# Kernel optimization log

Measured on AMD Instinct MI355X. Metric: run time of the kernel, lower is better.

Reference implementation:

```python
import jax, jax.numpy as jnp
import numpy as np

N, F, H, E, ES, G = 50000, 64, 4, 300000, 400000, 128
NS, EPS = 0.2, 1e-5  # LeakyReLU slope, BN eps


def setup_inputs() -> dict:
    k = jax.random.split(jax.random.key(0), 16)
    rn = lambda i, s, sc=1.0: jax.random.normal(k[i], s, jnp.float32) * sc
    return {
        "x": rn(0, (N, F)),
        "edge_index": jax.random.randint(k[1], (2, E), 0, N),
        "batch": jnp.sort(jax.random.randint(k[2], (N,), 0, G)),
        "scatter_edge_index": jax.random.randint(k[3], (4, 2, ES), 0, N),
        "scatter_edge_attr": rn(4, (4, ES), 0.1),
        "gat_W": rn(5, (4, F, H * F), 0.05),
        "gat_asrc": rn(6, (4, H, F), 0.05),
        "gat_adst": rn(7, (4, H, F), 0.05),
        "gat_bias": jnp.zeros((4, H * F)),
        "mlp_W": rn(8, (4, H * F, F), 0.05),
        "mlp_b": jnp.zeros((4, F)),
        "mlp_g": jnp.ones((4, F)), "mlp_beta": jnp.zeros((4, F)),
        "mlp_rm": jnp.zeros((4, F)), "mlp_rv": jax.random.uniform(k[9], (4, F)) + 0.5,
        "fc1_W": rn(10, (F, 256), 0.05), "fc1_b": jnp.zeros((256,)),
        "fc1_g": jnp.ones((256,)), "fc1_beta": jnp.zeros((256,)),
        "fc1_rm": jnp.zeros((256,)), "fc1_rv": jax.random.uniform(k[11], (256,)) + 0.5,
        "fc2_W": rn(12, (256, 64), 0.05), "fc2_b": jnp.zeros((64,)),
        "fc2_g": jnp.ones((64,)), "fc2_beta": jnp.zeros((64,)),
        "fc2_rm": jnp.zeros((64,)), "fc2_rv": jax.random.uniform(k[13], (64,)) + 0.5,
        "fc3_W": rn(14, (64, 10), 0.05), "fc3_b": jnp.zeros((10,)),
        "fc3_g": jnp.ones((10,)), "fc3_beta": jnp.zeros((10,)),
        "fc3_rm": jnp.zeros((10,)), "fc3_rv": jax.random.uniform(k[15], (10,)) + 0.5,
    }


def _bn(h, g, b, rm, rv):
    # BatchNorm1d in eval mode (running stats)
    return g * (h - rm) * jax.lax.rsqrt(rv + EPS) + b


def _forward(floats, ints):
    (x, sea, gW, gas, gad, gb, mW, mb, mg, mbe, mrm, mrv,
     f1W, f1b, f1g, f1be, f1rm, f1rv, f2W, f2b, f2g, f2be, f2rm, f2rv,
     f3W, f3b, f3g, f3be, f3rm, f3rv) = floats
    edge_index, batch, sei = ints
    n = x.shape[0]
    loop = jnp.arange(n)
    src = jnp.concatenate([edge_index[0], loop])  # GATConv adds self-loops
    dst = jnp.concatenate([edge_index[1], loop])

    def solo(i, h):
        # edge_attr-weighted scatter-add (solo_pass, aggr='add')
        s, t = sei[i, 0], sei[i, 1]
        return jax.ops.segment_sum(sea[i][:, None] * h[s], t, num_segments=n)

    def gat_mlp(i, h):
        hh = (h @ gW[i]).reshape(n, H, F)                       # [N,H,F]
        e = (hh * gas[i]).sum(-1)[src] + (hh * gad[i]).sum(-1)[dst]  # [E+N,H]
        e = jnp.where(e > 0, e, NS * e)                         # LeakyReLU(0.2)
        m = jax.ops.segment_max(e, dst, num_segments=n)         # segment softmax over dst
        ex = jnp.exp(e - m[dst])
        ssum = jax.ops.segment_sum(ex, dst, num_segments=n)
        alpha = ex / ssum[dst]
        out = jax.ops.segment_sum(hh[src] * alpha[:, :, None], dst, num_segments=n)
        out = out.reshape(n, H * F) + gb[i]                     # concat heads + bias
        h2 = jax.nn.elu(out) @ mW[i] + mb[i]                    # ELU -> Dropout(eval) -> Linear
        return _bn(h2, mg[i], mbe[i], mrm[i], mrv[i])

    x0 = solo(0, x)
    xh = [jnp.abs(solo(i, x)) for i in (1, 2, 3)]
    branches = [x0] + [solo(0, h) for h in xh]
    branches = [gat_mlp(i, branches[i]) for i in range(4)]
    x_stage2 = x + branches[0] + branches[1] + branches[2] + branches[3]
    pooled = jax.ops.segment_sum(x_stage2, batch, num_segments=G)   # global_add_pool
    h = jax.nn.relu(_bn(pooled @ f1W + f1b, f1g, f1be, f1rm, f1rv))
    h = jax.nn.relu(_bn(h @ f2W + f2b, f2g, f2be, f2rm, f2rv))
    return _bn(h @ f3W + f3b, f3g, f3be, f3rm, f3rv)  # [G, num_classes]


def reference(x, edge_index, batch, scatter_edge_index, scatter_edge_attr, gat_W, gat_asrc, gat_adst, gat_bias, mlp_W, mlp_b, mlp_g, mlp_beta, mlp_rm, mlp_rv, fc1_W, fc1_b, fc1_g, fc1_beta, fc1_rm, fc1_rv, fc2_W, fc2_b, fc2_g, fc2_beta, fc2_rm, fc2_rv, fc3_W, fc3_b, fc3_g, fc3_beta, fc3_rm, fc3_rv):
    floats = (x, scatter_edge_attr, gat_W, gat_asrc, gat_adst, gat_bias, mlp_W, mlp_b, mlp_g, mlp_beta, mlp_rm, mlp_rv, fc1_W, fc1_b, fc1_g, fc1_beta, fc1_rm, fc1_rv, fc2_W, fc2_b, fc2_g, fc2_beta, fc2_rm, fc2_rv, fc3_W, fc3_b, fc3_g, fc3_beta, fc3_rm, fc3_rv)
    return _forward(floats, (edge_index, batch, scatter_edge_index))
```

## Files before the change

### kernel.cpp

```cpp
#include <hip/hip_runtime.h>

typedef unsigned int uint;
typedef unsigned short u16;

#define NN 50000
#define FF 64
#define NHD 4
#define EE 300000
#define ESN 400000
#define NG 128
#define NSLOPE 0.2f
#define EPSBN 1e-5f

#define BINSZ 64
#define NBIN 782
#define NPOS (NBIN * BINSZ)
#define CHUNK 2048
#define NBLK 196
#define BST 40
#define BCAP 38

typedef float f32x4 __attribute__((ext_vector_type(4)));
typedef float f32x2 __attribute__((ext_vector_type(2)));
typedef short bf16x8 __attribute__((ext_vector_type(8)));
union U8 { uint4 u; bf16x8 s; };

static __device__ __forceinline__ float lrelu(float e) {
  return fmaxf(e, NSLOPE * e);
}
static __device__ __forceinline__ float bl(uint u) {
  return __uint_as_float(u << 16);
}
static __device__ __forceinline__ float bh(uint u) {
  return __uint_as_float(u & 0xFFFF0000u);
}
static __device__ __forceinline__ uint f2bf(float f) {
  uint u = __float_as_uint(f);
  return (u + 0x7FFFu + ((u >> 16) & 1u)) >> 16;
}
static __device__ __forceinline__ uint packbf(float a, float b) {
  return f2bf(a) | (f2bf(b) << 16);
}

__global__ __launch_bounds__(256) void k_setup(
    const float2* __restrict__ x, const float* __restrict__ gW,
    const float* __restrict__ gas, const float* __restrict__ gad,
    const float* __restrict__ mW, const float* __restrict__ mb,
    const float* __restrict__ mg, const float* __restrict__ mbe,
    const float* __restrict__ mrm, const float* __restrict__ mrv,
    uint* __restrict__ xbf, uint* __restrict__ WB2, float* __restrict__ wasd,
    uint* __restrict__ MB, float* __restrict__ cvec) {
  int i = blockIdx.x * 256 + threadIdx.x;
  if (i < NN * 32) {
    float2 v = x[i];
    xbf[i] = packbf(v.x, v.y);
  }
  int t = i;
  if (t < 8192) {
    int b = t >> 11, id = t & 2047;
    int h = id >> 9, r2 = id & 511;
    int q2 = r2 >> 8, r3 = r2 & 255;
    int ct = r3 >> 6, l = r3 & 63;
    int c = h * 64 + ct * 16 + (l & 15);
    int k0 = q2 * 32 + (l >> 4) * 8;
    const float* Wp = gW + b * 16384;
    uint4 o;
    o.x = packbf(Wp[(k0 + 0) * 256 + c], Wp[(k0 + 1) * 256 + c]);
    o.y = packbf(Wp[(k0 + 2) * 256 + c], Wp[(k0 + 3) * 256 + c]);
    o.z = packbf(Wp[(k0 + 4) * 256 + c], Wp[(k0 + 5) * 256 + c]);
    o.w = packbf(Wp[(k0 + 6) * 256 + c], Wp[(k0 + 7) * 256 + c]);
    ((uint4*)WB2)[t] = o;
  } else if (t < 8192 + 2048) {
    int id = t - 8192;
    int b = id >> 9, r = id & 511;
    int sd = r >> 8, r2 = r & 255;
    int h = r2 >> 6, k = r2 & 63;
    const float* Wp = gW + b * 16384;
    const float* ap = (sd ? gad : gas) + b * 256 + h * 64;
    float acc = 0.f;
    for (int f = 0; f < 64; ++f) acc += Wp[k * 256 + h * 64 + f] * ap[f];
    wasd[((b * 2 + sd) * 4 + h) * 64 + k] = acc;
  } else if (t < 8192 + 2048 + 8192) {
    int id = t - 10240;
    int b = id >> 11, rem = id & 2047;
    int tt = rem >> 6, l = rem & 63;
    int tile = tt >> 3, q2 = tt & 7;
    int c = tile * 16 + (l & 15);
    int k0 = q2 * 32 + (l >> 4) * 8;
    const float* Mp = mW + b * 16384;
    float sc = mg[b * 64 + c] * rsqrtf(mrv[b * 64 + c] + EPSBN);
    float v[8];
#pragma unroll
    for (int j = 0; j < 8; ++j) v[j] = Mp[(k0 + j) * 64 + c] * sc;
    uint4 o;
    o.x = packbf(v[0], v[1]); o.y = packbf(v[2], v[3]);
    o.z = packbf(v[4], v[5]); o.w = packbf(v[6], v[7]);
    ((uint4*)MB)[id] = o;
  } else if (t < 8192 + 2048 + 8192 + 64) {
    int c = t - 18432;
    float acc = 0.f;
#pragma unroll
    for (int b = 0; b < 4; ++b) {
      float sc = mg[b * 64 + c] * rsqrtf(mrv[b * 64 + c] + EPSBN);
      acc += sc * (mb[b * 64 + c] - mrm[b * 64 + c]) + mbe[b * 64 + c];
    }
    cvec[c] = acc;
  }
}

__global__ __launch_bounds__(256) void k_sort1(
    const int* __restrict__ sei, const float* __restrict__ sea,
    const int* __restrict__ ei, uint2* __restrict__ sorted,
    u16* __restrict__ offs) {
  __shared__ uint hist[NBIN];
  __shared__ uint wsum[4];
  __shared__ __align__(16) uint2 buf[CHUNK];
  int y = blockIdx.y, blk = blockIdx.x, tid = threadIdx.x;
  int E = (y < 4) ? ESN : EE;
  int e0 = blk * CHUNK;
  if (e0 >= E) return;
  int ec = E - e0; if (ec > CHUNK) ec = CHUNK;
  for (int i = tid; i < NBIN; i += 256) hist[i] = 0;
  __syncthreads();
  const int* sptr; const int* tptr; const float* wptr = 0;
  if (y < 4) {
    sptr = sei + (size_t)y * 2 * ESN; tptr = sptr + ESN;
    wptr = sea + (size_t)y * ESN;
  } else {
    sptr = ei; tptr = ei + EE;
  }
  uint2 rec[8]; uint rbin[8];
#pragma unroll
  for (int k = 0; k < 8; ++k) {
    int idx = tid + k * 256;
    rbin[k] = 0xFFFFFFFFu;
    if (idx < ec) {
      int e = e0 + idx;
      int s = sptr[e], t = tptr[e];
      uint w = (y < 4) ? (f2bf(wptr[e]) << 16) : 0u;
      rec[k].x = (uint)s | ((uint)(t & 63) << 16);
      rec[k].y = w;
      rbin[k] = (uint)(t >> 6);
      atomicAdd(&hist[rbin[k]], 1u);
    }
  }
  __syncthreads();
  int t4 = tid * 4;
  uint h0 = 0, h1 = 0, h2 = 0, h3 = 0;
  if (t4 + 0 < NBIN) h0 = hist[t4 + 0];
  if (t4 + 1 < NBIN) h1 = hist[t4 + 1];
  if (t4 + 2 < NBIN) h2 = hist[t4 + 2];
  if (t4 + 3 < NBIN) h3 = hist[t4 + 3];
  uint sl = h0 + h1 + h2 + h3;
  uint pre = sl;
#pragma unroll
  for (int off = 1; off < 64; off <<= 1) {
    uint nv = __shfl_up(pre, off);
    if ((tid & 63) >= off) pre += nv;
  }
  int wid = tid >> 6;
  if ((tid & 63) == 63) wsum[wid] = pre;
  __syncthreads();
  uint wbase = 0;
#pragma unroll
  for (int w = 0; w < 4; ++w) if (w < wid) wbase += wsum[w];
  uint base = wbase + pre - sl;
  if (t4 + 0 < NBIN) hist[t4 + 0] = base;
  if (t4 + 1 < NBIN) hist[t4 + 1] = base + h0;
  if (t4 + 2 < NBIN) hist[t4 + 2] = base + h0 + h1;
  if (t4 + 3 < NBIN) hist[t4 + 3] = base + h0 + h1 + h2;
  __syncthreads();
  u16* ob = offs + ((size_t)y * NBLK + blk) * 784;
  for (int i = tid; i < NBIN; i += 256) ob[i] = (u16)hist[i];
  if (tid == 0) { ob[NBIN] = (u16)ec; ob[NBIN + 1] = (u16)ec; }
  __syncthreads();
#pragma unroll
  for (int k = 0; k < 8; ++k) {
    if (rbin[k] != 0xFFFFFFFFu) {
      uint p = atomicAdd(&hist[rbin[k]], 1u);
      buf[p] = rec[k];
    }
  }
  __syncthreads();
  uint2* sb = sorted + ((size_t)y * NBLK + blk) * CHUNK;
  uint4* s4 = (uint4*)sb;
  const uint4* b4 = (const uint4*)buf;
  int n4 = (ec + 1) >> 1;
  for (int i = tid; i < n4; i += 256) s4[i] = b4[i];
}

__global__ __launch_bounds__(256) void k_sort2(
    const u16* __restrict__ offs, const uint2* __restrict__ sorted,
    uint* __restrict__ pbk, uint* __restrict__ gbk) {
  __shared__ __align__(16) uint Lb[BINSZ * BST];
  __shared__ uint Lc[BINSZ];
  __shared__ uint dh[64], dpos[64], sperm[64];
  int y = blockIdx.y, bin = blockIdx.x, tid = threadIdx.x;
  if (tid < BINSZ) Lc[tid] = 0u;
  if (tid < 64) dh[tid] = 0u;
  __syncthreads();
  int nblk = (y < 4) ? NBLK : 147;
  for (int sb = tid; sb < nblk; sb += 256) {
    const u16* ob = offs + ((size_t)y * NBLK + sb) * 784;
    uint st = ob[bin], en = ob[bin + 1];
    const uint2* src = sorted + ((size_t)y * NBLK + sb) * CHUNK;
    for (uint i = st; i < en; ++i) {
      uint2 r = src[i];
      uint tl = (r.x >> 16) & 63u;
      uint p = atomicAdd(&Lc[tl], 1u);
      if (p < BCAP) Lb[tl * BST + 2 + p] = (r.x & 0xFFFFu) | r.y;
    }
  }
  __syncthreads();
  uint myd = 0;
  if (tid < 64) {
    myd = Lc[tid]; if (myd > 63u) myd = 63u;
    atomicAdd(&dh[63u - myd], 1u);
  }
  __syncthreads();
  if (tid < 64) {
    uint v = dh[tid], p = v;
#pragma unroll
    for (int off = 1; off < 64; off <<= 1) {
      uint nv = __shfl_up(p, off);
      if (tid >= off) p += nv;
    }
    dpos[tid] = p - v;
  }
  __syncthreads();
  if (tid < 64) {
    uint slot = atomicAdd(&dpos[63u - myd], 1u);
    sperm[slot] = (uint)tid;
    Lb[tid * BST + 0] = Lc[tid];
    Lb[tid * BST + 1] = (uint)(bin * BINSZ + tid);
  }
  __syncthreads();
  uint* out = (y < 4) ? (pbk + ((size_t)y * NPOS + (size_t)bin * BINSZ) * BST)
                      : (gbk + (size_t)bin * BINSZ * BST);
  uint4* o4v = (uint4*)out;
  for (int i = tid; i < 64 * (BST / 4); i += 256) {
    int pos = i / (BST / 4), q = i % (BST / 4);
    uint sn = sperm[pos];
    uint4 v = *(const uint4*)&Lb[sn * BST + q * 4];
    o4v[(size_t)pos * (BST / 4) + q] = v;
  }
}

__global__ __launch_bounds__(256) void k_solo_gA(
    const uint* __restrict__ xbf, const uint* __restrict__ pbk,
    const float* __restrict__ wasd, uint* __restrict__ bbuf,
    uint* __restrict__ tmpb, float* __restrict__ es4,
    float* __restrict__ ed4) {
  int i = blockIdx.y;
  int tid = threadIdx.x;
  int pos = blockIdx.x * 32 + (tid >> 3);
  int sl = tid & 7;
  const uint* bk = pbk + ((size_t)i * NPOS + pos) * BST;
  int deg = (int)bk[0]; deg = deg > BCAP ? BCAP : deg;
  int id = (int)bk[1];
  if (id >= NN) return;
  const uint* pp = bk + 2;
  f32x2 A0 = {0.f, 0.f}, A1 = {0.f, 0.f}, A2 = {0.f, 0.f}, A3 = {0.f, 0.f};
  for (int j = 0; j < deg; j += 8) {
    uint2 pa = *(const uint2*)&pp[j];
    uint2 pb = *(const uint2*)&pp[j + 2];
    uint2 pc = *(const uint2*)&pp[j + 4];
    uint2 pd = *(const uint2*)&pp[j + 6];
    uint p0 = pa.x;
    uint p1 = (j + 1 < deg) ? pa.y : 0u;
    uint p2 = (j + 2 < deg) ? pb.x : 0u;
    uint p3 = (j + 3 < deg) ? pb.y : 0u;
    uint p4 = (j + 4 < deg) ? pc.x : 0u;
    uint p5 = (j + 5 < deg) ? pc.y : 0u;
    uint p6 = (j + 6 < deg) ? pd.x : 0u;
    uint p7 = (j + 7 < deg) ? pd.y : 0u;
    uint4 v0 = *(const uint4*)&xbf[(size_t)(p0 & 0xFFFFu) * 32 + sl * 4];
    uint4 v1 = *(const uint4*)&xbf[(size_t)(p1 & 0xFFFFu) * 32 + sl * 4];
    uint4 v2 = *(const uint4*)&xbf[(size_t)(p2 & 0xFFFFu) * 32 + sl * 4];
    uint4 v3 = *(const uint4*)&xbf[(size_t)(p3 & 0xFFFFu) * 32 + sl * 4];
    uint4 v4 = *(const uint4*)&xbf[(size_t)(p4 & 0xFFFFu) * 32 + sl * 4];
    uint4 v5 = *(const uint4*)&xbf[(size_t)(p5 & 0xFFFFu) * 32 + sl * 4];
    uint4 v6 = *(const uint4*)&xbf[(size_t)(p6 & 0xFFFFu) * 32 + sl * 4];
    uint4 v7 = *(const uint4*)&xbf[(size_t)(p7 & 0xFFFFu) * 32 + sl * 4];
#define SOLOA_EDGE(V, W)                              \
    {                                                 \
      float w_ = (W);                                 \
      f32x2 w2_ = {w_, w_};                           \
      A0 += (f32x2){bl(V.x), bh(V.x)} * w2_;          \
      A1 += (f32x2){bl(V.y), bh(V.y)} * w2_;          \
      A2 += (f32x2){bl(V.z), bh(V.z)} * w2_;          \
      A3 += (f32x2){bl(V.w), bh(V.w)} * w2_;          \
    }
    SOLOA_EDGE(v0, bh(p0));
    SOLOA_EDGE(v1, bh(p1));
    SOLOA_EDGE(v2, bh(p2));
    SOLOA_EDGE(v3, bh(p3));
    SOLOA_EDGE(v4, bh(p4));
    SOLOA_EDGE(v5, bh(p5));
    SOLOA_EDGE(v6, bh(p6));
    SOLOA_EDGE(v7, bh(p7));
#undef SOLOA_EDGE
  }
  uint4 o;
  o.x = packbf(A0[0], A0[1]); o.y = packbf(A1[0], A1[1]);
  o.z = packbf(A2[0], A2[1]); o.w = packbf(A3[0], A3[1]);
  if (i == 0) {
    *(uint4*)&bbuf[(size_t)id * 32 + sl * 4] = o;
  } else {
    *(uint4*)&tmpb[(size_t)id * 96 + (size_t)(i - 1) * 32 + sl * 4] = o;
  }
  if (i == 0) {
    float pv[8] = {A0[0], A0[1], A1[0], A1[1], A2[0], A2[1], A3[0], A3[1]};
    const float* wa = wasd;
    float r[8];
#pragma unroll
    for (int o8 = 0; o8 < 8; ++o8) {
      const float* w8 = wa + o8 * 64 + sl * 8;
      float a = 0.f;
#pragma unroll
      for (int j = 0; j < 8; ++j) a += pv[j] * w8[j];
      r[o8] = a;
    }
#pragma unroll
    for (int off = 1; off < 8; off <<= 1)
#pragma unroll
      for (int o8 = 0; o8 < 8; ++o8) r[o8] += __shfl_xor(r[o8], off);
    if (sl == 0) {
      *(float4*)&es4[(size_t)id * 4] = make_float4(r[0], r[1], r[2], r[3]);
      *(float4*)&ed4[(size_t)id * 4] = make_float4(r[4], r[5], r[6], r[7]);
    }
  }
}

__global__ __launch_bounds__(256) void k_solo_gB(
    const uint* __restrict__ tmpb, const uint* __restrict__ pbk,
    const float* __restrict__ wasd, uint* __restrict__ bbuf,
    float* __restrict__ es4, float* __restrict__ ed4) {
  int tid = threadIdx.x;
  int pos = blockIdx.x * 32 + (tid >> 3);
  int sl = tid & 7;
  const uint* bk = pbk + (size_t)pos * BST;
  int deg = (int)bk[0]; deg = deg > BCAP ? BCAP : deg;
  int id = (int)bk[1];
  if (id >= NN) return;
  const uint* pp = bk + 2;
  f32x2 A[3][4];
#pragma unroll
  for (int k = 0; k < 3; ++k)
#pragma unroll
    for (int c = 0; c < 4; ++c) A[k][c] = (f32x2){0.f, 0.f};
  for (int j = 0; j < deg; j += 4) {
    uint2 pa = *(const uint2*)&pp[j];
    uint2 pb = *(const uint2*)&pp[j + 2];
    uint p0 = pa.x;
    uint p1 = (j + 1 < deg) ? pa.y : 0u;
    uint p2 = (j + 2 < deg) ? pb.x : 0u;
    uint p3 = (j + 3 < deg) ? pb.y : 0u;
    const uint* b0 = &tmpb[(size_t)(p0 & 0xFFFFu) * 96 + sl * 4];
    const uint* b1 = &tmpb[(size_t)(p1 & 0xFFFFu) * 96 + sl * 4];
    const uint* b2 = &tmpb[(size_t)(p2 & 0xFFFFu) * 96 + sl * 4];
    const uint* b3 = &tmpb[(size_t)(p3 & 0xFFFFu) * 96 + sl * 4];
    uint4 v00 = *(const uint4*)&b0[0];
    uint4 v01 = *(const uint4*)&b0[32];
    uint4 v02 = *(const uint4*)&b0[64];
    uint4 v10 = *(const uint4*)&b1[0];
    uint4 v11 = *(const uint4*)&b1[32];
    uint4 v12 = *(const uint4*)&b1[64];
    uint4 v20 = *(const uint4*)&b2[0];
    uint4 v21 = *(const uint4*)&b2[32];
    uint4 v22 = *(const uint4*)&b2[64];
    uint4 v30 = *(const uint4*)&b3[0];
    uint4 v31 = *(const uint4*)&b3[32];
    uint4 v32 = *(const uint4*)&b3[64];
    float w0 = bh(p0), w1 = bh(p1), w2 = bh(p2), w3 = bh(p3);
    f32x2 w20 = {w0, w0}, w21 = {w1, w1}, w22 = {w2, w2}, w23 = {w3, w3};
#define SOLOB_EDGE(K, V, W)                                       \
    {                                                             \
      A[K][0] += (f32x2){fabsf(bl(V.x)), fabsf(bh(V.x))} * (W);   \
      A[K][1] += (f32x2){fabsf(bl(V.y)), fabsf(bh(V.y))} * (W);   \
      A[K][2] += (f32x2){fabsf(bl(V.z)), fabsf(bh(V.z))} * (W);   \
      A[K][3] += (f32x2){fabsf(bl(V.w)), fabsf(bh(V.w))} * (W);   \
    }
    SOLOB_EDGE(0, v00, w20); SOLOB_EDGE(1, v01, w20); SOLOB_EDGE(2, v02, w20);
    SOLOB_EDGE(0, v10, w21); SOLOB_EDGE(1, v11, w21); SOLOB_EDGE(2, v12, w21);
    SOLOB_EDGE(0, v20, w22); SOLOB_EDGE(1, v21, w22); SOLOB_EDGE(2, v22, w22);
    SOLOB_EDGE(0, v30, w23); SOLOB_EDGE(1, v31, w23); SOLOB_EDGE(2, v32, w23);
#undef SOLOB_EDGE
  }
#pragma unroll
  for (int k = 0; k < 3; ++k) {
    int b = k + 1;
    uint4 o;
    o.x = packbf(A[k][0][0], A[k][0][1]); o.y = packbf(A[k][1][0], A[k][1][1]);
    o.z = packbf(A[k][2][0], A[k][2][1]); o.w = packbf(A[k][3][0], A[k][3][1]);
    *(uint4*)&bbuf[(size_t)b * NN * 32 + (size_t)id * 32 + sl * 4] = o;
    float pv[8] = {A[k][0][0], A[k][0][1], A[k][1][0], A[k][1][1],
                   A[k][2][0], A[k][2][1], A[k][3][0], A[k][3][1]};
    const float* wa = wasd + b * 512;
    float r[8];
#pragma unroll
    for (int o8 = 0; o8 < 8; ++o8) {
      const float* w8 = wa + o8 * 64 + sl * 8;
      float a = 0.f;
#pragma unroll
      for (int j = 0; j < 8; ++j) a += pv[j] * w8[j];
      r[o8] = a;
    }
#pragma unroll
    for (int off = 1; off < 8; off <<= 1)
#pragma unroll
      for (int o8 = 0; o8 < 8; ++o8) r[o8] += __shfl_xor(r[o8], off);
    if (sl == 0) {
      *(float4*)&es4[(size_t)b * NN * 4 + (size_t)id * 4] =
          make_float4(r[0], r[1], r[2], r[3]);
      *(float4*)&ed4[(size_t)b * NN * 4 + (size_t)id * 4] =
          make_float4(r[4], r[5], r[6], r[7]);
    }
  }
}

__global__ __launch_bounds__(256) void k_agg(
    const uint* __restrict__ gbk, const float* __restrict__ es4,
    const float* __restrict__ ed4, const uint* __restrict__ bbuf,
    uint* __restrict__ agg4) {
  __shared__ uint gbr[32][40];
  __shared__ uint2 meta[32][32];
  int br = blockIdx.y;
  const float4* es44 = (const float4*)(es4 + (size_t)br * NN * 4);
  const float4* ed44 = (const float4*)(ed4 + (size_t)br * NN * 4);
  const uint* bbf = bbuf + (size_t)br * NN * 32;
  int tid = threadIdx.x;
  int p0 = blockIdx.x * 32;
  for (int idx = tid; idx < 320; idx += 256) {
    int i = idx / 10, q = idx % 10;
    *(uint4*)&gbr[i][q * 4] =
        *(const uint4*)&gbk[((size_t)p0 + i) * BST + q * 4];
  }
  __syncthreads();
  {
    int g = tid >> 5, hl = tid & 31;
#pragma unroll
    for (int rep = 0; rep < 4; ++rep) {
      int i = rep * 8 + g;
      int id = (int)gbr[i][1];
      bool vld = id < NN;
      int nds = vld ? id : 0;
      int deg = vld ? (int)gbr[i][0] : 0;
      deg = deg > 31 ? 31 : deg;
      int s0 = (hl < deg) ? (int)gbr[i][2 + hl] : nds;
      bool act = hl <= deg;
      float4 edd = ed44[nds];
      float4 e4 = es44[s0];
      float val[4];
      val[0] = act ? lrelu(e4.x + edd.x) : -3e38f;
      val[1] = act ? lrelu(e4.y + edd.y) : -3e38f;
      val[2] = act ? lrelu(e4.z + edd.z) : -3e38f;
      val[3] = act ? lrelu(e4.w + edd.w) : -3e38f;
      float m[4] = {val[0], val[1], val[2], val[3]};
#pragma unroll
      for (int off = 1; off < 32; off <<= 1)
#pragma unroll
        for (int h = 0; h < 4; ++h) m[h] = fmaxf(m[h], __shfl_xor(m[h], off));
      float e[4], sm[4];
#pragma unroll
      for (int h = 0; h < 4; ++h) {
        e[h] = act ? __expf(val[h] - m[h]) : 0.f;
        sm[h] = e[h];
      }
#pragma unroll
      for (int off = 1; off < 32; off <<= 1)
#pragma unroll
        for (int h = 0; h < 4; ++h) sm[h] += __shfl_xor(sm[h], off);
      float inv[4];
#pragma unroll
      for (int h = 0; h < 4; ++h) inv[h] = __builtin_amdgcn_rcpf(sm[h]);
      meta[i][hl] = make_uint2(packbf(e[0] * inv[0], e[1] * inv[1]),
                               packbf(e[2] * inv[2], e[3] * inv[3]));
    }
  }
  __syncthreads();
  {
    int wv = tid >> 6, l = tid & 63;
    int i = wv * 8 + (l >> 3), sl = l & 7;
    int id = (int)gbr[i][1];
    bool vld = id < NN;
    int self = vld ? id : 0;
    int deg = vld ? (int)gbr[i][0] : 0;
    deg = deg > 31 ? 31 : deg;
    int tot = deg + 1;
    f32x2 a00={0.f,0.f},a01={0.f,0.f},a02={0.f,0.f},a03={0.f,0.f};
    f32x2 a10={0.f,0.f},a11={0.f,0.f},a12={0.f,0.f},a13={0.f,0.f};
    f32x2 a20={0.f,0.f},a21={0.f,0.f},a22={0.f,0.f},a23={0.f,0.f};
    f32x2 a30={0.f,0.f},a31={0.f,0.f},a32={0.f,0.f},a33={0.f,0.f};
    for (int j = 0; j < tot; j += 4) {
      int s0 = (j     < deg) ? (int)gbr[i][2 + j]  : self;
      int s1 = (j + 1 < deg) ? (int)gbr[i][3 + j]  : self;
      int s2 = (j + 2 < deg) ? (int)gbr[i][4 + j]  : self;
      int s3 = (j + 3 < deg) ? (int)gbr[i][5 + j]  : self;
      uint2 al0 = meta[i][j];
      uint2 al1 = meta[i][j + 1];
      uint2 al2 = meta[i][j + 2];
      uint2 al3 = meta[i][j + 3];
      uint4 v0 = *(const uint4*)&bbf[(size_t)s0 * 32 + sl * 4];
      uint4 v1 = *(const uint4*)&bbf[(size_t)s1 * 32 + sl * 4];
      uint4 v2 = *(const uint4*)&bbf[(size_t)s2 * 32 + sl * 4];
      uint4 v3 = *(const uint4*)&bbf[(size_t)s3 * 32 + sl * 4];
#define AGG_EDGE(V, AL)                                              \
      {                                                              \
        f32x2 w0_={bl(AL.x),bl(AL.x)}, w1_={bh(AL.x),bh(AL.x)};      \
        f32x2 w2_={bl(AL.y),bl(AL.y)}, w3_={bh(AL.y),bh(AL.y)};      \
        f32x2 p0_={bl(V.x),bh(V.x)}, p1_={bl(V.y),bh(V.y)};          \
        f32x2 p2_={bl(V.z),bh(V.z)}, p3_={bl(V.w),bh(V.w)};          \
        a00+=p0_*w0_; a01+=p1_*w0_; a02+=p2_*w0_; a03+=p3_*w0_;      \
        a10+=p0_*w1_; a11+=p1_*w1_; a12+=p2_*w1_; a13+=p3_*w1_;      \
        a20+=p0_*w2_; a21+=p1_*w2_; a22+=p2_*w2_; a23+=p3_*w2_;      \
        a30+=p0_*w3_; a31+=p1_*w3_; a32+=p2_*w3_; a33+=p3_*w3_;      \
      }
      AGG_EDGE(v0, al0);
      AGG_EDGE(v1, al1);
      AGG_EDGE(v2, al2);
      AGG_EDGE(v3, al3);
#undef AGG_EDGE
    }
    if (vld) {
      uint* outp = agg4 + ((size_t)br * NN + id) * 128;
      uint4 o;
      o.x=packbf(a00[0],a00[1]); o.y=packbf(a01[0],a01[1]);
      o.z=packbf(a02[0],a02[1]); o.w=packbf(a03[0],a03[1]);
      *(uint4*)&outp[0 * 32 + sl * 4] = o;
      o.x=packbf(a10[0],a10[1]); o.y=packbf(a11[0],a11[1]);
      o.z=packbf(a12[0],a12[1]); o.w=packbf(a13[0],a13[1]);
      *(uint4*)&outp[1 * 32 + sl * 4] = o;
      o.x=packbf(a20[0],a20[1]); o.y=packbf(a21[0],a21[1]);
      o.z=packbf(a22[0],a22[1]); o.w=packbf(a23[0],a23[1]);
      *(uint4*)&outp[2 * 32 + sl * 4] = o;
      o.x=packbf(a30[0],a30[1]); o.y=packbf(a31[0],a31[1]);
      o.z=packbf(a32[0],a32[1]); o.w=packbf(a33[0],a33[1]);
      *(uint4*)&outp[3 * 32 + sl * 4] = o;
    }
  }
}

__global__ __launch_bounds__(256) void k_mlp2(
    const uint* __restrict__ agg4, const uint* __restrict__ WB2,
    const uint* __restrict__ MB4, const float* __restrict__ gb,
    const float* __restrict__ cvec, const float* __restrict__ xsrc,
    float* __restrict__ xs2) {
  __shared__ union UU2 {
    struct {
      uint astg[32][128];
      uint elu[4][32][32];
    } s;
    float red[4][32][64];
  } u;
  int tid = threadIdx.x, wv = tid >> 6, l = tid & 63;
  int quad = l >> 4, m16 = l & 15;
  int n0 = blockIdx.x * 32;
  int h = wv;
  f32x4 macc[2][4] = {{{0.f,0.f,0.f,0.f},{0.f,0.f,0.f,0.f},
                       {0.f,0.f,0.f,0.f},{0.f,0.f,0.f,0.f}},
                      {{0.f,0.f,0.f,0.f},{0.f,0.f,0.f,0.f},
                       {0.f,0.f,0.f,0.f},{0.f,0.f,0.f,0.f}}};
  u16* eluw = (u16*)&u.s.elu[wv][0][0];
  for (int br = 0; br < 4; ++br) {
    if (br) __syncthreads();
    {
      const uint* src = agg4 + ((size_t)br * NN + n0) * 128;
      for (int i2 = tid; i2 < 4096; i2 += 256) {
        int row = i2 >> 7, col = i2 & 127;
        u.s.astg[row][col ^ ((row & 7) << 2)] = src[i2];
      }
    }
    __syncthreads();
    uint4 Bh[2][4];
#pragma unroll
    for (int kk = 0; kk < 2; ++kk)
#pragma unroll
      for (int ct = 0; ct < 4; ++ct)
        Bh[kk][ct] =
            ((const uint4*)WB2)[(((br * 4 + h) * 2 + kk) * 4 + ct) * 64 + l];
#pragma unroll
    for (int mt = 0; mt < 2; ++mt) {
      int row = mt * 16 + m16;
      const uint* ar = &u.s.astg[row][0];
      int sw = (row & 7) << 2;
      U8 a0, a1;
      a0.u = *(const uint4*)&ar[(h * 32 + quad * 4) ^ sw];
      a1.u = *(const uint4*)&ar[(h * 32 + 16 + quad * 4) ^ sw];
#pragma unroll
      for (int ct = 0; ct < 4; ++ct) {
        f32x4 acc = {0.f, 0.f, 0.f, 0.f};
        U8 b0, b1; b0.u = Bh[0][ct]; b1.u = Bh[1][ct];
        acc = __builtin_amdgcn_mfma_f32_16x16x32_bf16(a0.s, b0.s, acc, 0, 0, 0);
        acc = __builtin_amdgcn_mfma_f32_16x16x32_bf16(a1.s, b1.s, acc, 0, 0, 0);
        float gbv = gb[br * 256 + h * 64 + ct * 16 + m16];
#pragma unroll
        for (int r = 0; r < 4; ++r) {
          float v = acc[r] + gbv;
          v = v > 0.f ? v : (__expf(v) - 1.f);
          int erow = mt * 16 + quad * 4 + r;
          int ucs = ((ct * 16 + m16) >> 1) ^ ((erow & 7) << 2);
          eluw[(erow * 32 + ucs) * 2 + (m16 & 1)] = (u16)f2bf(v);
        }
      }
    }
    const uint4* MBb = (const uint4*)MB4 + br * 2048;
    uint4 Bm[4][2];
#pragma unroll
    for (int t = 0; t < 4; ++t)
#pragma unroll
      for (int kk = 0; kk < 2; ++kk)
        Bm[t][kk] = MBb[(t * 8 + wv * 2 + kk) * 64 + l];
#pragma unroll
    for (int mt = 0; mt < 2; ++mt) {
      int row = mt * 16 + m16;
      int sw = (row & 7) << 2;
      const uint* er = &u.s.elu[wv][row][0];
      U8 a0, a1;
      a0.u = *(const uint4*)&er[(quad * 4) ^ sw];
      a1.u = *(const uint4*)&er[(16 + quad * 4) ^ sw];
#pragma unroll
      for (int t = 0; t < 4; ++t) {
        U8 b0, b1; b0.u = Bm[t][0]; b1.u = Bm[t][1];
        macc[mt][t] =
            __builtin_amdgcn_mfma_f32_16x16x32_bf16(a0.s, b0.s, macc[mt][t], 0, 0, 0);
        macc[mt][t] =
            __builtin_amdgcn_mfma_f32_16x16x32_bf16(a1.s, b1.s, macc[mt][t], 0, 0, 0);
      }
    }
  }
  __syncthreads();
#pragma unroll
  for (int mt = 0; mt < 2; ++mt)
#pragma unroll
    for (int t = 0; t < 4; ++t)
#pragma unroll
      for (int r = 0; r < 4; ++r)
        u.red[wv][mt * 16 + quad * 4 + r][t * 16 + m16] = macc[mt][t][r];
  __syncthreads();
  for (int e = tid; e < 2048; e += 256) {
    int node = e >> 6, col = e & 63;
    int nd = n0 + node;
    if (nd < NN) {
      float v = u.red[0][node][col] + u.red[1][node][col] +
                u.red[2][node][col] + u.red[3][node][col];
      size_t idx = (size_t)nd * 64 + col;
      xs2[idx] = xsrc[idx] + v + cvec[col];
    }
  }
}

__global__ __launch_bounds__(512) void k_poolhead(
    const float* __restrict__ xs2, const int* __restrict__ batch,
    const float* __restrict__ f1W, const float* __restrict__ f1b,
    const float* __restrict__ f1g, const float* __restrict__ f1be,
    const float* __restrict__ f1rm, const float* __restrict__ f1rv,
    const float* __restrict__ f2W, const float* __restrict__ f2b,
    const float* __restrict__ f2g, const float* __restrict__ f2be,
    const float* __restrict__ f2rm, const float* __restrict__ f2rv,
    const float* __restrict__ f3W, const float* __restrict__ f3b,
    const float* __restrict__ f3g, const float* __restrict__ f3be,
    const float* __restrict__ f3rm, const float* __restrict__ f3rv,
    float* __restrict__ out) {
  __shared__ float p[64], h1[256], h2[64], red[8][64];
  int g = blockIdx.x, tid = threadIdx.x;
  int wv = tid >> 6, lane = tid & 63;
  int lo = 0, hi = NN;
  while (lo < hi) { int mid = (lo + hi) >> 1; if (batch[mid] < g) lo = mid + 1; else hi = mid; }
  int beg = lo;
  lo = 0; hi = NN;
  while (lo < hi) { int mid = (lo + hi) >> 1; if (batch[mid] < g + 1) lo = mid + 1; else hi = mid; }
  int end = lo;
  float acc = 0.f;
  for (int n = beg + wv; n < end; n += 8) acc += xs2[(size_t)n * FF + lane];
  red[wv][lane] = acc;
  __syncthreads();
  if (tid < 64) {
    float s = 0.f;
#pragma unroll
    for (int w = 0; w < 8; ++w) s += red[w][tid];
    p[tid] = s;
  }
  __syncthreads();
  if (tid < 256) {
    float a = f1b[tid];
    for (int k = 0; k < 64; ++k) a += p[k] * f1W[k * 256 + tid];
    a = f1g[tid] * (a - f1rm[tid]) * rsqrtf(f1rv[tid] + EPSBN) + f1be[tid];
    h1[tid] = a > 0.f ? a : 0.f;
  }
  __syncthreads();
  if (tid < 64) {
    float b = f2b[tid];
    for (int k = 0; k < 256; ++k) b += h1[k] * f2W[k * 64 + tid];
    b = f2g[tid] * (b - f2rm[tid]) * rsqrtf(f2rv[tid] + EPSBN) + f2be[tid];
    h2[tid] = b > 0.f ? b : 0.f;
  }
  __syncthreads();
  if (tid < 10) {
    float c = f3b[tid];
    for (int k = 0; k < 64; ++k) c += h2[k] * f3W[k * 10 + tid];
    c = f3g[tid] * (c - f3rm[tid]) * rsqrtf(f3rv[tid] + EPSBN) + f3be[tid];
    out[g * 10 + tid] = c;
  }
}

extern "C" void kernel_launch(void* const* d_in, const int* in_sizes, int n_in,
                              void* d_out, int out_size, void* d_ws,
                              size_t ws_size, hipStream_t stream) {
  const float* x     = (const float*)d_in[0];
  const int*   ei    = (const int*)d_in[1];
  const int*   batch = (const int*)d_in[2];
  const int*   sei   = (const int*)d_in[3];
  const float* sea   = (const float*)d_in[4];
  const float* gW    = (const float*)d_in[5];
  const float* gas   = (const float*)d_in[6];
  const float* gad   = (const float*)d_in[7];
  const float* gb    = (const float*)d_in[8];
  const float* mW    = (const float*)d_in[9];
  const float* mb    = (const float*)d_in[10];
  const float* mg    = (const float*)d_in[11];
  const float* mbe   = (const float*)d_in[12];
  const float* mrm   = (const float*)d_in[13];
  const float* mrv   = (const float*)d_in[14];
  const float* f1W   = (const float*)d_in[15];
  const float* f1b   = (const float*)d_in[16];
  const float* f1g   = (const float*)d_in[17];
  const float* f1be  = (const float*)d_in[18];
  const float* f1rm  = (const float*)d_in[19];
  const float* f1rv  = (const float*)d_in[20];
  const float* f2W   = (const float*)d_in[21];
  const float* f2b   = (const float*)d_in[22];
  const float* f2g   = (const float*)d_in[23];
  const float* f2be  = (const float*)d_in[24];
  const float* f2rm  = (const float*)d_in[25];
  const float* f2rv  = (const float*)d_in[26];
  const float* f3W   = (const float*)d_in[27];
  const float* f3b   = (const float*)d_in[28];
  const float* f3g   = (const float*)d_in[29];
  const float* f3be  = (const float*)d_in[30];
  const float* f3rm  = (const float*)d_in[31];
  const float* f3rv  = (const float*)d_in[32];
  float* out = (float*)d_out;

  char* base = (char*)d_ws;
  float* xs2 = (float*)base;
  uint* gbk  = (uint*)(base + (size_t)NN * 64 * 4);
  uint* xbf  = gbk + (size_t)NPOS * BST;
  uint* bbuf = xbf + (size_t)NN * 32;
  uint* tmpb = bbuf + (size_t)4 * NN * 32;
  uint* pbk  = tmpb + (size_t)NN * 96;
  uint2* sorted = (uint2*)(pbk + (size_t)4 * NPOS * BST);
  u16* offs = (u16*)(sorted + (size_t)5 * NBLK * CHUNK);
  uint* agg4 = (uint*)(offs + (size_t)5 * NBLK * 784);
  float* es4 = (float*)(agg4 + ((size_t)4 * NN + 32) * 128);
  float* ed4 = es4 + (size_t)4 * NN * 4;
  float* cvec = ed4 + (size_t)4 * NN * 4;
  float* wasd = cvec + 64;
  uint* WB2 = (uint*)(wasd + 2048);
  uint* MB4 = WB2 + 4 * 8192;

  size_t need = (size_t)((char*)(MB4 + 4 * 8192) - base);
  if (ws_size < need) return;

  k_setup<<<(NN * 32 + 255) / 256, 256, 0, stream>>>(
      (const float2*)x, gW, gas, gad, mW, mb, mg, mbe, mrm, mrv, xbf, WB2,
      wasd, MB4, cvec);

  dim3 gS1(NBLK, 5);
  k_sort1<<<gS1, 256, 0, stream>>>(sei, sea, ei, sorted, offs);
  dim3 gS2(NBIN, 5);
  k_sort2<<<gS2, 256, 0, stream>>>(offs, sorted, pbk, gbk);

  dim3 gA(NPOS / 32, 4);
  k_solo_gA<<<gA, 256, 0, stream>>>(xbf, pbk, wasd, bbuf, tmpb, es4, ed4);
  k_solo_gB<<<NPOS / 32, 256, 0, stream>>>(tmpb, pbk, wasd, bbuf, es4, ed4);

  dim3 gAg(NPOS / 32, 4);
  k_agg<<<gAg, 256, 0, stream>>>(gbk, es4, ed4, bbuf, agg4);
  k_mlp2<<<(NN + 31) / 32, 256, 0, stream>>>(agg4, WB2, MB4, gb, cvec, x, xs2);

  k_poolhead<<<NG, 512, 0, stream>>>(xs2, batch, f1W, f1b, f1g, f1be, f1rm,
                                     f1rv, f2W, f2b, f2g, f2be, f2rm, f2rv,
                                     f3W, f3b, f3g, f3be, f3rm, f3rv, out);
}
```

Before: 378.2 us.

## Store aggregation output in MFMA-fragment tile layout and load fragments directly

k_agg now writes its bf16 aggregated features into a per-32-node tiled layout that matches the MFMA A-fragment order, so k_mlp2 reads its A operands straight from global memory instead of staging a 32x128 tile through swizzled LDS with barriers each branch. This removes the LDS staging copy and two syncthreads per branch and shrinks shared memory use. Separately, the attention coefficients in k_agg's meta buffer are kept as fp32 float4 (padded to 33 columns) instead of packed bf16, skipping the unpack ops at the cost of more LDS space and bandwidth. The scattered 16-byte writes in k_agg may coalesce less well than the old row-contiguous stores.

```diff
diff --git a/kernel.cpp b/kernel.cpp
--- a/kernel.cpp
+++ b/kernel.cpp
@@ -19,6 +19,8 @@
 #define NBLK 196
 #define BST 40
 #define BCAP 38
+#define NTIL 1563
+#define AGGST ((size_t)NTIL * 4096)
 
 typedef float f32x4 __attribute__((ext_vector_type(4)));
 typedef float f32x2 __attribute__((ext_vector_type(2)));
@@ -424,7 +426,7 @@
     const float* __restrict__ ed4, const uint* __restrict__ bbuf,
     uint* __restrict__ agg4) {
   __shared__ uint gbr[32][40];
-  __shared__ uint2 meta[32][32];
+  __shared__ float4 meta[32][33];
   int br = blockIdx.y;
   const float4* es44 = (const float4*)(es4 + (size_t)br * NN * 4);
   const float4* ed44 = (const float4*)(ed4 + (size_t)br * NN * 4);
@@ -474,8 +476,8 @@
       float inv[4];
 #pragma unroll
       for (int h = 0; h < 4; ++h) inv[h] = __builtin_amdgcn_rcpf(sm[h]);
-      meta[i][hl] = make_uint2(packbf(e[0] * inv[0], e[1] * inv[1]),
-                               packbf(e[2] * inv[2], e[3] * inv[3]));
+      meta[i][hl] = make_float4(e[0] * inv[0], e[1] * inv[1], e[2] * inv[2],
+                                e[3] * inv[3]);
     }
   }
   __syncthreads();
@@ -497,22 +499,22 @@
       int s1 = (j + 1 < deg) ? (int)gbr[i][3 + j]  : self;
       int s2 = (j + 2 < deg) ? (int)gbr[i][4 + j]  : self;
       int s3 = (j + 3 < deg) ? (int)gbr[i][5 + j]  : self;
-      uint2 al0 = meta[i][j];
-      uint2 al1 = meta[i][j + 1];
-      uint2 al2 = meta[i][j + 2];
-      uint2 al3 = meta[i][j + 3];
+      float4 al0 = meta[i][j];
+      float4 al1 = meta[i][j + 1];
+      float4 al2 = meta[i][j + 2];
+      float4 al3 = meta[i][j + 3];
       uint4 v0 = *(const uint4*)&bbf[(size_t)s0 * 32 + sl * 4];
       uint4 v1 = *(const uint4*)&bbf[(size_t)s1 * 32 + sl * 4];
       uint4 v2 = *(const uint4*)&bbf[(size_t)s2 * 32 + sl * 4];
       uint4 v3 = *(const uint4*)&bbf[(size_t)s3 * 32 + sl * 4];
 #define AGG_EDGE(V, AL)                                              \
       {                                                              \
-        f32x2 w0_={bl(AL.x),bl(AL.x)}, w1_={bh(AL.x),bh(AL.x)};      \
-        f32x2 w2_={bl(AL.y),bl(AL.y)}, w3_={bh(AL.y),bh(AL.y)};      \
+        f32x2 w0_={AL.x,AL.x}, w1_={AL.y,AL.y};                      \
+        f32x2 w2_={AL.z,AL.z}, w3_={AL.w,AL.w};                      \
         f32x2 p0_={bl(V.x),bh(V.x)}, p1_={bl(V.y),bh(V.y)};          \
         f32x2 p2_={bl(V.z),bh(V.z)}, p3_={bl(V.w),bh(V.w)};          \
         a00+=p0_*w0_; a01+=p1_*w0_; a02+=p2_*w0_; a03+=p3_*w0_;      \
-        a10+=p0_*w1_; a11+=p1_*w1_; a12+=p2_*w1_; a13+=p3_*w1_;      \
+        a10+=p0_*w1_; a11+=p1_*w1_; a12+=p2_*w1_; a13+=p3_*w1_;     \
         a20+=p0_*w2_; a21+=p1_*w2_; a22+=p2_*w2_; a23+=p3_*w2_;      \
         a30+=p0_*w3_; a31+=p1_*w3_; a32+=p2_*w3_; a33+=p3_*w3_;      \
       }
@@ -523,20 +525,21 @@
 #undef AGG_EDGE
     }
     if (vld) {
-      uint* outp = agg4 + ((size_t)br * NN + id) * 128;
+      int t = id >> 5, i32 = id & 31;
+      uint* outp = agg4 + (size_t)br * AGGST + (size_t)t * 4096;
       uint4 o;
       o.x=packbf(a00[0],a00[1]); o.y=packbf(a01[0],a01[1]);
       o.z=packbf(a02[0],a02[1]); o.w=packbf(a03[0],a03[1]);
-      *(uint4*)&outp[0 * 32 + sl * 4] = o;
+      *(uint4*)&outp[(((0 * 8 + sl) * 32) + i32) * 4] = o;
       o.x=packbf(a10[0],a10[1]); o.y=packbf(a11[0],a11[1]);
       o.z=packbf(a12[0],a12[1]); o.w=packbf(a13[0],a13[1]);
-      *(uint4*)&outp[1 * 32 + sl * 4] = o;
+      *(uint4*)&outp[(((1 * 8 + sl) * 32) + i32) * 4] = o;
       o.x=packbf(a20[0],a20[1]); o.y=packbf(a21[0],a21[1]);
       o.z=packbf(a22[0],a22[1]); o.w=packbf(a23[0],a23[1]);
-      *(uint4*)&outp[2 * 32 + sl * 4] = o;
+      *(uint4*)&outp[(((2 * 8 + sl) * 32) + i32) * 4] = o;
       o.x=packbf(a30[0],a30[1]); o.y=packbf(a31[0],a31[1]);
       o.z=packbf(a32[0],a32[1]); o.w=packbf(a33[0],a33[1]);
-      *(uint4*)&outp[3 * 32 + sl * 4] = o;
+      *(uint4*)&outp[(((3 * 8 + sl) * 32) + i32) * 4] = o;
     }
   }
 }
@@ -547,10 +550,7 @@
     const float* __restrict__ cvec, const float* __restrict__ xsrc,
     float* __restrict__ xs2) {
   __shared__ union UU2 {
-    struct {
-      uint astg[32][128];
-      uint elu[4][32][32];
-    } s;
+    uint elu[4][32][32];
     float red[4][32][64];
   } u;
   int tid = threadIdx.x, wv = tid >> 6, l = tid & 63;
@@ -561,17 +561,9 @@
                        {0.f,0.f,0.f,0.f},{0.f,0.f,0.f,0.f}},
                       {{0.f,0.f,0.f,0.f},{0.f,0.f,0.f,0.f},
                        {0.f,0.f,0.f,0.f},{0.f,0.f,0.f,0.f}}};
-  u16* eluw = (u16*)&u.s.elu[wv][0][0];
+  u16* eluw = (u16*)&u.elu[wv][0][0];
   for (int br = 0; br < 4; ++br) {
-    if (br) __syncthreads();
-    {
-      const uint* src = agg4 + ((size_t)br * NN + n0) * 128;
-      for (int i2 = tid; i2 < 4096; i2 += 256) {
-        int row = i2 >> 7, col = i2 & 127;
-        u.s.astg[row][col ^ ((row & 7) << 2)] = src[i2];
-      }
-    }
-    __syncthreads();
+    const uint* ap = agg4 + (size_t)br * AGGST + (size_t)blockIdx.x * 4096;
     uint4 Bh[2][4];
 #pragma unroll
     for (int kk = 0; kk < 2; ++kk)
@@ -581,12 +573,10 @@
             ((const uint4*)WB2)[(((br * 4 + h) * 2 + kk) * 4 + ct) * 64 + l];
 #pragma unroll
     for (int mt = 0; mt < 2; ++mt) {
-      int row = mt * 16 + m16;
-      const uint* ar = &u.s.astg[row][0];
-      int sw = (row & 7) << 2;
+      int i32 = mt * 16 + m16;
       U8 a0, a1;
-      a0.u = *(const uint4*)&ar[(h * 32 + quad * 4) ^ sw];
-      a1.u = *(const uint4*)&ar[(h * 32 + 16 + quad * 4) ^ sw];
+      a0.u = *(const uint4*)&ap[(((h * 8 + quad) * 32) + i32) * 4];
+      a1.u = *(const uint4*)&ap[(((h * 8 + quad + 4) * 32) + i32) * 4];
 #pragma unroll
       for (int ct = 0; ct < 4; ++ct) {
         f32x4 acc = {0.f, 0.f, 0.f, 0.f};
@@ -615,7 +605,7 @@
     for (int mt = 0; mt < 2; ++mt) {
       int row = mt * 16 + m16;
       int sw = (row & 7) << 2;
-      const uint* er = &u.s.elu[wv][row][0];
+      const uint* er = &u.elu[wv][row][0];
       U8 a0, a1;
       a0.u = *(const uint4*)&er[(quad * 4) ^ sw];
       a1.u = *(const uint4*)&er[(16 + quad * 4) ^ sw];
@@ -752,7 +742,7 @@
   uint2* sorted = (uint2*)(pbk + (size_t)4 * NPOS * BST);
   u16* offs = (u16*)(sorted + (size_t)5 * NBLK * CHUNK);
   uint* agg4 = (uint*)(offs + (size_t)5 * NBLK * 784);
-  float* es4 = (float*)(agg4 + ((size_t)4 * NN + 32) * 128);
+  float* es4 = (float*)(agg4 + (size_t)4 * AGGST);
   float* ed4 = es4 + (size_t)4 * NN * 4;
   float* cvec = ed4 + (size_t)4 * NN * 4;
   float* wasd = cvec + 64;
@@ -777,7 +767,7 @@
 
   dim3 gAg(NPOS / 32, 4);
   k_agg<<<gAg, 256, 0, stream>>>(gbk, es4, ed4, bbuf, agg4);
-  k_mlp2<<<(NN + 31) / 32, 256, 0, stream>>>(agg4, WB2, MB4, gb, cvec, x, xs2);
+  k_mlp2<<<NTIL, 256, 0, stream>>>(agg4, WB2, MB4, gb, cvec, x, xs2);
 
   k_poolhead<<<NG, 512, 0, stream>>>(xs2, batch, f1W, f1b, f1g, f1be, f1rm,
                                      f1rv, f2W, f2b, f2g, f2be, f2rm, f2rv,
```

Measured after the change: 399.7 us. +5.7%, slower.
